# Kernel optimization log

Hardware: AMD Instinct MI355X
Metric: run time of the kernel (lower is better)

## Reference

```python
import jax, jax.numpy as jnp
import numpy as np

SIZE = 11
SIGMA = 1.5
C1 = 0.01 ** 2
C2 = 0.03 ** 2


def gaussian_kernel(size, sigma):
    x, y = np.mgrid[-size:size + 1, -size:size + 1]
    k = np.exp(-0.5 * (x * x + y * y) / (sigma * sigma))
    return (k / k.sum()).astype(np.float32)


def _dwconv(x, w, pad):
    # depthwise conv, NCHW input, OIHW kernel (C,1,kh,kw)
    return jax.lax.conv_general_dilated(
        x, w, window_strides=(1, 1), padding=[(pad, pad), (pad, pad)],
        dimension_numbers=('NCHW', 'OIHW', 'NCHW'),
        feature_group_count=x.shape[1])


def setup_inputs() -> dict:
    key = jax.random.key(0)
    k1, k2 = jax.random.split(key)
    B, C, H, W = 16, 3, 512, 512
    inp = jax.random.uniform(k1, (B, C, H, W), dtype=jnp.float32)
    tgt = jax.random.uniform(k2, (B, C, H, W), dtype=jnp.float32)
    kern = gaussian_kernel(SIZE, SIGMA)  # (23,23)
    weight = jnp.asarray(np.tile(kern, (C, 1, 1, 1)))  # (C,1,23,23)
    return {"input": inp, "target": tgt, "weight": weight}


def reference(input, target, weight):
    pad = SIZE
    mean1 = _dwconv(input, weight, pad)
    mean2 = _dwconv(target, weight, pad)
    mean1_sq = mean1 * mean1
    mean2_sq = mean2 * mean2
    mean_12 = mean1 * mean2
    sigma1_sq = _dwconv(input * input, weight, pad) - mean1_sq
    sigma2_sq = _dwconv(target * target, weight, pad) - mean2_sq
    sigma_12 = _dwconv(input * target, weight, pad) - mean_12
    ssim = (2 * mean_12 + C1) * (2 * sigma_12 + C2) / (
        (mean1_sq + mean2_sq + C1) * (sigma1_sq + sigma2_sq + C2))
    return 1.0 - ssim.mean()
```

## Files before the change

kernel.cpp:

```cpp
#include <hip/hip_runtime.h>
#include <hip/hip_bf16.h>

typedef float f32x4 __attribute__((ext_vector_type(4)));
typedef short bf16x8 __attribute__((ext_vector_type(8)));

#define HH 512
#define WW 512
#define NPLANES 48
#define KSIZE 23
#define NBLK (16 * 16 * NPLANES)
#define C1V 1.0e-4f
#define C2V 9.0e-4f

#define SB_O   0
#define SA_O   3960
#define OV_O   7920
#define G_O    8568
#define HB_O   0
#define HB_CH  2048
#define SPITCH 72
#define LDS_TOT 10616

#define SWZ(rho, k) ((k) ^ (((rho) & 7) << 3))

__device__ __forceinline__ unsigned cvtpk(float a, float b) {
    union { __hip_bfloat162 h; unsigned u; } cv;
    cv.h = __float22bfloat162_rn(make_float2(a, b));
    return cv.u;
}

__device__ __forceinline__ void prod2(unsigned a, unsigned b,
                                      unsigned& pab, unsigned& pss) {
    float al = __uint_as_float(a << 16), ah = __uint_as_float(a & 0xffff0000u);
    float bl = __uint_as_float(b << 16), bh = __uint_as_float(b & 0xffff0000u);
    pab = cvtpk(al * bl, ah * bh);
    pss = cvtpk(al * al + bl * bl, ah * ah + bh * bh);
}

__device__ __forceinline__ f32x4 mfma16(uint4 a, uint4 b, f32x4 c) {
    union { uint4 u; bf16x8 h; } ua, ub;
    ua.u = a; ub.u = b;
    return __builtin_amdgcn_mfma_f32_16x16x32_bf16(ua.h, ub.h, c, 0, 0, 0);
}

__global__ __launch_bounds__(64) void ssim_prep_kernel(
    const float* __restrict__ w, unsigned* __restrict__ Gg)
{
    const int lane = threadIdx.x;
    float gv = 0.f;
    if (lane < KSIZE) {
        #pragma unroll
        for (int k = 0; k < KSIZE; ++k) gv += w[lane * KSIZE + k];
    }
    for (int idx = lane; idx < 32 * 32; idx += 64) {
        int r = idx >> 5, kd = idx & 31;
        int d0 = 2 * kd - 1 - r;
        float g0 = __shfl(gv, d0 & 63, 64);
        float g1 = __shfl(gv, (d0 + 1) & 63, 64);
        g0 = ((unsigned)d0 < (unsigned)KSIZE) ? g0 : 0.f;
        g1 = ((unsigned)(d0 + 1) < (unsigned)KSIZE) ? g1 : 0.f;
        Gg[idx] = cvtpk(g0, g1);
    }
}

__global__ __launch_bounds__(256, 6) void ssim_main_kernel(
    const float* __restrict__ in, const float* __restrict__ tg,
    const unsigned* __restrict__ Gg, float* __restrict__ partial)
{
    __shared__ __align__(16) unsigned short lds[LDS_TOT];
    __shared__ float swsum[4];

    const int tid = threadIdx.x;
    const int wave = tid >> 6, lane = tid & 63;
    const int m = lane & 15, q = lane >> 4;

    const int blk = blockIdx.x;
    const int plane = blk >> 8;
    const int t2 = blk & 255;
    const int x0 = (t2 & 15) * 32 - 12;
    const int y0 = (t2 >> 4) * 32 - 12;
    const float* __restrict__ inp = in + (size_t)plane * (HH * WW);
    const float* __restrict__ tgp = tg + (size_t)plane * (HH * WW);

    const bool interior = (x0 >= 0) && (y0 >= 0) && (x0 + 64 <= WW) && (y0 + 55 <= HH);

    float4 La[2][2], Lb[2][2];
    if (interior) {
        #pragma unroll
        for (int it = 0; it < 2; ++it) {
            int t = tid + it * 256;
            if (t < 440) {
                int r = t >> 3, c8 = (t & 7) << 3;
                const float4* pa = (const float4*)(inp + (y0 + r) * WW + x0 + c8);
                const float4* pb = (const float4*)(tgp + (y0 + r) * WW + x0 + c8);
                La[it][0] = pa[0]; La[it][1] = pa[1];
                Lb[it][0] = pb[0]; Lb[it][1] = pb[1];
            }
        }
    }

    {
        int r = tid >> 3;
        int dc = (tid & 7) << 2;
        uint4 g4 = *(const uint4*)(Gg + r * 32 + dc);
        *(uint4*)&lds[G_O + r * 64 + (((dc << 1)) ^ ((r & 7) << 3))] = g4;
    }
    if (tid < 81) {
        uint4 z; z.x = z.y = z.z = z.w = 0u;
        *(uint4*)&lds[OV_O + tid * 8] = z;
    }

    if (interior) {
        #pragma unroll
        for (int it = 0; it < 2; ++it) {
            int t = tid + it * 256;
            if (t < 440) {
                int r = t >> 3, c8 = (t & 7) << 3;
                uint4 va, vb;
                va.x = cvtpk(La[it][0].x, La[it][0].y); va.y = cvtpk(La[it][0].z, La[it][0].w);
                va.z = cvtpk(La[it][1].x, La[it][1].y); va.w = cvtpk(La[it][1].z, La[it][1].w);
                vb.x = cvtpk(Lb[it][0].x, Lb[it][0].y); vb.y = cvtpk(Lb[it][0].z, Lb[it][0].w);
                vb.z = cvtpk(Lb[it][1].x, Lb[it][1].y); vb.w = cvtpk(Lb[it][1].z, Lb[it][1].w);
                *(uint4*)&lds[SA_O + r * SPITCH + c8] = va;
                *(uint4*)&lds[SB_O + r * SPITCH + c8] = vb;
            }
        }
    } else {
        unsigned* ldsw = (unsigned*)lds;
        for (int t = tid; t < 55 * 32; t += 256) {
            int r = t >> 5, cd = t & 31;
            int gy = y0 + r, gx = x0 + cd * 2;
            float a0 = 0.f, a1 = 0.f, b0 = 0.f, b1 = 0.f;
            if (gy >= 0 && gy < HH) {
                const float* ri = inp + gy * WW;
                const float* rt = tgp + gy * WW;
                if ((unsigned)gx < (unsigned)WW)       { a0 = ri[gx];     b0 = rt[gx]; }
                if ((unsigned)(gx + 1) < (unsigned)WW) { a1 = ri[gx + 1]; b1 = rt[gx + 1]; }
            }
            ldsw[(SA_O >> 1) + r * 36 + cd] = cvtpk(a0, a1);
            ldsw[(SB_O >> 1) + r * 36 + cd] = cvtpk(b0, b1);
        }
    }
    __syncthreads();

    f32x4 acc[4][2];
    const f32x4 zz = {0.f, 0.f, 0.f, 0.f};
    #pragma unroll
    for (int ch = 0; ch < 4; ++ch) { acc[ch][0] = zz; acc[ch][1] = zz; }

    #pragma unroll
    for (int ks = 0; ks < 2; ++ks) {
        const int off = (wave * 16 + m) * SPITCH + ks * 32 + q * 8;
        uint4 ua = *(const uint4*)&lds[SA_O + off];
        uint4 ub = *(const uint4*)&lds[SB_O + off];
        uint4 uab, uss;
        prod2(ua.x, ub.x, uab.x, uss.x);
        prod2(ua.y, ub.y, uab.y, uss.y);
        prod2(ua.z, ub.z, uab.z, uss.z);
        prod2(ua.w, ub.w, uab.w, uss.w);
        #pragma unroll
        for (int nc = 0; nc < 2; ++nc) {
            const int gr = nc * 16 + m;
            uint4 gf = *(const uint4*)&lds[G_O + gr * 64 + SWZ(gr, ks * 32 + q * 8)];
            acc[0][nc] = mfma16(ua,  gf, acc[0][nc]);
            acc[1][nc] = mfma16(ub,  gf, acc[1][nc]);
            acc[2][nc] = mfma16(uss, gf, acc[2][nc]);
            acc[3][nc] = mfma16(uab, gf, acc[3][nc]);
        }
    }
    __syncthreads();

    #pragma unroll
    for (int ch = 0; ch < 4; ++ch)
        #pragma unroll
        for (int nc = 0; nc < 2; ++nc) {
            f32x4 a = acc[ch][nc];
            uint2 pk;
            pk.x = cvtpk(a[0], a[1]);
            pk.y = cvtpk(a[2], a[3]);
            const int col = nc * 16 + m;
            const int rb = wave * 16 + q * 4;
            *(uint2*)&lds[HB_O + ch * HB_CH + col * 64 + SWZ(col, rb)] = pk;
        }
    __syncthreads();

    const int mrow = wave >> 1, nc2 = wave & 1;
    f32x4 av[4];
    #pragma unroll
    for (int ch = 0; ch < 4; ++ch) av[ch] = zz;

    #pragma unroll
    for (int ks = 0; ks < 2; ++ks) {
        const int ar = mrow * 16 + m;
        uint4 ga = *(const uint4*)&lds[G_O + ar * 64 + SWZ(ar, ks * 32 + q * 8)];
        #pragma unroll
        for (int ch = 0; ch < 4; ++ch) {
            const int col = nc2 * 16 + m;
            uint4 ub = *(const uint4*)&lds[HB_O + ch * HB_CH + col * 64 + SWZ(col, ks * 32 + q * 8)];
            av[ch] = mfma16(ga, ub, av[ch]);
        }
    }

    float lsum = 0.f;
    #pragma unroll
    for (int i = 0; i < 4; ++i) {
        float vx = av[0][i], vt = av[1][i];
        float vss = av[2][i], vxt = av[3][i];
        float m1s = vx * vx, m2s = vt * vt, m12 = vx * vt;
        float sss = vss - m1s - m2s;
        float s12 = vxt - m12;
        float num = (2.f * m12 + C1V) * (2.f * s12 + C2V);
        float den = (m1s + m2s + C1V) * (sss + C2V);
        lsum += num * __builtin_amdgcn_rcpf(den);
    }
    #pragma unroll
    for (int off = 32; off > 0; off >>= 1)
        lsum += __shfl_down(lsum, off, 64);
    if (lane == 0) swsum[wave] = lsum;
    __syncthreads();
    if (tid == 0)
        partial[blk] = swsum[0] + swsum[1] + swsum[2] + swsum[3];
}

__global__ __launch_bounds__(256) void ssim_final_kernel(
    const float* __restrict__ partial, float* __restrict__ out)
{
    __shared__ float swsum[4];
    const int tid = threadIdx.x;
    float s = 0.f;
    const float4* p4 = (const float4*)partial;
    for (int i = tid; i < NBLK / 4; i += 256) {
        float4 v = p4[i];
        s += (v.x + v.y) + (v.z + v.w);
    }
    #pragma unroll
    for (int off = 32; off > 0; off >>= 1)
        s += __shfl_down(s, off, 64);
    if ((tid & 63) == 0) swsum[tid >> 6] = s;
    __syncthreads();
    if (tid == 0)
        out[0] = 1.0f - (swsum[0] + swsum[1] + swsum[2] + swsum[3])
                        * (1.0f / ((float)NPLANES * HH * WW));
}

extern "C" void kernel_launch(void* const* d_in, const int* in_sizes, int n_in,
                              void* d_out, int out_size, void* d_ws, size_t ws_size,
                              hipStream_t stream) {
    const float* inp = (const float*)d_in[0];
    const float* tgt = (const float*)d_in[1];
    const float* wgt = (const float*)d_in[2];
    float* out = (float*)d_out;
    float* partial = (float*)d_ws;
    unsigned* Gg = (unsigned*)((char*)d_ws + NBLK * sizeof(float));

    ssim_prep_kernel<<<1, 64, 0, stream>>>(wgt, Gg);
    ssim_main_kernel<<<NBLK, 256, 0, stream>>>(inp, tgt, Gg, partial);
    ssim_final_kernel<<<1, 256, 0, stream>>>(partial, out);
}
```

Before: 157.5 us.

## Fold prep and final reduction kernels into main kernel with atomic last-block reduce

Each block now builds the packed Gaussian weight table in LDS directly from the 23x23 weight tensor instead of reading a table made by a separate prep kernel. The final reduction moves into the main kernel: every block bumps an atomic counter, and the last block to finish sums all partials and writes the result. This drops two kernel launches but adds a memset launch, 23-element weight row sums in every block, and a threadfence plus atomic per block.

```diff
diff --git a/kernel.cpp b/kernel.cpp
--- a/kernel.cpp
+++ b/kernel.cpp
@@ -43,32 +43,14 @@
     return __builtin_amdgcn_mfma_f32_16x16x32_bf16(ua.h, ub.h, c, 0, 0, 0);
 }
 
-__global__ __launch_bounds__(64) void ssim_prep_kernel(
-    const float* __restrict__ w, unsigned* __restrict__ Gg)
-{
-    const int lane = threadIdx.x;
-    float gv = 0.f;
-    if (lane < KSIZE) {
-        #pragma unroll
-        for (int k = 0; k < KSIZE; ++k) gv += w[lane * KSIZE + k];
-    }
-    for (int idx = lane; idx < 32 * 32; idx += 64) {
-        int r = idx >> 5, kd = idx & 31;
-        int d0 = 2 * kd - 1 - r;
-        float g0 = __shfl(gv, d0 & 63, 64);
-        float g1 = __shfl(gv, (d0 + 1) & 63, 64);
-        g0 = ((unsigned)d0 < (unsigned)KSIZE) ? g0 : 0.f;
-        g1 = ((unsigned)(d0 + 1) < (unsigned)KSIZE) ? g1 : 0.f;
-        Gg[idx] = cvtpk(g0, g1);
-    }
-}
-
 __global__ __launch_bounds__(256, 6) void ssim_main_kernel(
     const float* __restrict__ in, const float* __restrict__ tg,
-    const unsigned* __restrict__ Gg, float* __restrict__ partial)
+    const float* __restrict__ w, float* __restrict__ partial,
+    int* __restrict__ counter, float* __restrict__ out)
 {
     __shared__ __align__(16) unsigned short lds[LDS_TOT];
     __shared__ float swsum[4];
+    __shared__ int lastFlag;
 
     const int tid = threadIdx.x;
     const int wave = tid >> 6, lane = tid & 63;
@@ -100,10 +82,24 @@
     }
 
     {
-        int r = tid >> 3;
-        int dc = (tid & 7) << 2;
-        uint4 g4 = *(const uint4*)(Gg + r * 32 + dc);
-        *(uint4*)&lds[G_O + r * 64 + (((dc << 1)) ^ ((r & 7) << 3))] = g4;
+        float gv = 0.f;
+        if (lane < KSIZE) {
+            #pragma unroll
+            for (int k = 0; k < KSIZE; ++k) gv += w[lane * KSIZE + k];
+        }
+        unsigned* gw = (unsigned*)lds + (G_O >> 1);
+        const int kd = lane & 31;
+        const int rh = (lane >> 5) << 2;
+        #pragma unroll
+        for (int i = 0; i < 4; ++i) {
+            int r = wave * 8 + rh + i;
+            int d0 = 2 * kd - 1 - r;
+            float g0 = __shfl(gv, d0 & 63, 64);
+            float g1 = __shfl(gv, (d0 + 1) & 63, 64);
+            g0 = ((unsigned)d0 < (unsigned)KSIZE) ? g0 : 0.f;
+            g1 = ((unsigned)(d0 + 1) < (unsigned)KSIZE) ? g1 : 0.f;
+            gw[r * 32 + (kd ^ ((r & 7) << 2))] = cvtpk(g0, g1);
+        }
     }
     if (tid < 81) {
         uint4 z; z.x = z.y = z.z = z.w = 0u;
@@ -218,29 +214,32 @@
         lsum += __shfl_down(lsum, off, 64);
     if (lane == 0) swsum[wave] = lsum;
     __syncthreads();
-    if (tid == 0)
+
+    if (tid == 0) {
         partial[blk] = swsum[0] + swsum[1] + swsum[2] + swsum[3];
-}
-
-__global__ __launch_bounds__(256) void ssim_final_kernel(
-    const float* __restrict__ partial, float* __restrict__ out)
-{
-    __shared__ float swsum[4];
-    const int tid = threadIdx.x;
-    float s = 0.f;
-    const float4* p4 = (const float4*)partial;
-    for (int i = tid; i < NBLK / 4; i += 256) {
-        float4 v = p4[i];
-        s += (v.x + v.y) + (v.z + v.w);
-    }
-    #pragma unroll
-    for (int off = 32; off > 0; off >>= 1)
-        s += __shfl_down(s, off, 64);
-    if ((tid & 63) == 0) swsum[tid >> 6] = s;
-    __syncthreads();
-    if (tid == 0)
-        out[0] = 1.0f - (swsum[0] + swsum[1] + swsum[2] + swsum[3])
-                        * (1.0f / ((float)NPLANES * HH * WW));
+        __threadfence();
+        int old = atomicAdd(counter, 1);
+        lastFlag = (old == NBLK - 1);
+    }
+    __syncthreads();
+    if (lastFlag) {
+        __threadfence();
+        float s = 0.f;
+        const float4* p4 = (const float4*)partial;
+        for (int i = tid; i < NBLK / 4; i += 256) {
+            float4 v = p4[i];
+            s += (v.x + v.y) + (v.z + v.w);
+        }
+        #pragma unroll
+        for (int off = 32; off > 0; off >>= 1)
+            s += __shfl_down(s, off, 64);
+        __syncthreads();
+        if (lane == 0) swsum[wave] = s;
+        __syncthreads();
+        if (tid == 0)
+            out[0] = 1.0f - (swsum[0] + swsum[1] + swsum[2] + swsum[3])
+                            * (1.0f / ((float)NPLANES * HH * WW));
+    }
 }
 
 extern "C" void kernel_launch(void* const* d_in, const int* in_sizes, int n_in,
@@ -251,9 +250,9 @@
     const float* wgt = (const float*)d_in[2];
     float* out = (float*)d_out;
     float* partial = (float*)d_ws;
-    unsigned* Gg = (unsigned*)((char*)d_ws + NBLK * sizeof(float));
-
-    ssim_prep_kernel<<<1, 64, 0, stream>>>(wgt, Gg);
-    ssim_main_kernel<<<NBLK, 256, 0, stream>>>(inp, tgt, Gg, partial);
-    ssim_final_kernel<<<1, 256, 0, stream>>>(partial, out);
-}
+    int* counter = (int*)((char*)d_ws + NBLK * sizeof(float));
+
+    hipMemsetAsync(counter, 0, sizeof(int), stream);
+    ssim_main_kernel<<<NBLK, 256, 0, stream>>>(inp, tgt, wgt, partial,
+                                               counter, out);
+}
```

Measured after the change: 581.2 us. +269.1%, slower.

## Widen output tile to 64x32 per block with 512 threads

Applied to the files above, without the earlier changes.

Each block now computes a 64-wide by 32-tall output tile using 8 waves instead of a 32x32 tile with 4 waves, which halves the block count. The horizontal halo overhead per output drops because a 96-column input strip (12-pixel halo on each side) is loaded for 64 output columns instead of a 64-column strip for 32. The Gaussian band matrix grows to 64x96, and its XOR swizzle is replaced by a padded pitch. The cost is more LDS per block (about 46 KB) and larger blocks, which may lower occupancy and the number of blocks resident per CU.

```diff
diff --git a/kernel.cpp b/kernel.cpp
--- a/kernel.cpp
+++ b/kernel.cpp
@@ -8,18 +8,19 @@
 #define WW 512
 #define NPLANES 48
 #define KSIZE 23
-#define NBLK (16 * 16 * NPLANES)
+#define NBLK (8 * 16 * NPLANES)
 #define C1V 1.0e-4f
 #define C2V 9.0e-4f
 
-#define SB_O   0
-#define SA_O   3960
-#define OV_O   7920
-#define G_O    8568
-#define HB_O   0
-#define HB_CH  2048
-#define SPITCH 72
-#define LDS_TOT 10616
+#define G_O    0
+#define SB_O   6656
+#define SA_O   12376
+#define OV_O   18096
+#define HB_O   6656
+#define HB_CH  4096
+#define SPITCH 104
+#define SROWS  55
+#define LDS_TOT 23040
 
 #define SWZ(rho, k) ((k) ^ (((rho) & 7) << 3))
 
@@ -43,92 +44,109 @@
     return __builtin_amdgcn_mfma_f32_16x16x32_bf16(ua.h, ub.h, c, 0, 0, 0);
 }
 
-__global__ __launch_bounds__(64) void ssim_prep_kernel(
+__global__ __launch_bounds__(256) void ssim_prep_kernel(
     const float* __restrict__ w, unsigned* __restrict__ Gg)
 {
-    const int lane = threadIdx.x;
+    const int tid = threadIdx.x, lane = tid & 63;
     float gv = 0.f;
     if (lane < KSIZE) {
         #pragma unroll
         for (int k = 0; k < KSIZE; ++k) gv += w[lane * KSIZE + k];
     }
-    for (int idx = lane; idx < 32 * 32; idx += 64) {
-        int r = idx >> 5, kd = idx & 31;
-        int d0 = 2 * kd - 1 - r;
-        float g0 = __shfl(gv, d0 & 63, 64);
-        float g1 = __shfl(gv, (d0 + 1) & 63, 64);
-        g0 = ((unsigned)d0 < (unsigned)KSIZE) ? g0 : 0.f;
-        g1 = ((unsigned)(d0 + 1) < (unsigned)KSIZE) ? g1 : 0.f;
-        Gg[idx] = cvtpk(g0, g1);
-    }
-}
-
-__global__ __launch_bounds__(256, 6) void ssim_main_kernel(
+    const int idx = blockIdx.x * 256 + tid;
+    const int r = idx / 48, kd = idx % 48;
+    const int d0 = 2 * kd - 1 - r;
+    float g0 = __shfl(gv, d0 & 63, 64);
+    float g1 = __shfl(gv, (d0 + 1) & 63, 64);
+    g0 = ((unsigned)d0 < (unsigned)KSIZE) ? g0 : 0.f;
+    g1 = ((unsigned)(d0 + 1) < (unsigned)KSIZE) ? g1 : 0.f;
+    Gg[r * 48 + kd] = cvtpk(g0, g1);
+}
+
+__global__ __launch_bounds__(512, 6) void ssim_main_kernel(
     const float* __restrict__ in, const float* __restrict__ tg,
     const unsigned* __restrict__ Gg, float* __restrict__ partial)
 {
     __shared__ __align__(16) unsigned short lds[LDS_TOT];
-    __shared__ float swsum[4];
+    __shared__ float swsum[8];
 
     const int tid = threadIdx.x;
     const int wave = tid >> 6, lane = tid & 63;
     const int m = lane & 15, q = lane >> 4;
 
     const int blk = blockIdx.x;
-    const int plane = blk >> 8;
-    const int t2 = blk & 255;
-    const int x0 = (t2 & 15) * 32 - 12;
-    const int y0 = (t2 >> 4) * 32 - 12;
+    const int plane = blk >> 7;
+    const int t2 = blk & 127;
+    const int tx = t2 & 7, ty = t2 >> 3;
+    const int x0 = tx * 64 - 12;
+    const int y0 = ty * 32 - 12;
     const float* __restrict__ inp = in + (size_t)plane * (HH * WW);
     const float* __restrict__ tgp = tg + (size_t)plane * (HH * WW);
 
-    const bool interior = (x0 >= 0) && (y0 >= 0) && (x0 + 64 <= WW) && (y0 + 55 <= HH);
+    const bool interior = (x0 >= 0) && (y0 >= 0) &&
+                          (x0 + 96 <= WW) && (y0 + SROWS <= HH);
 
     float4 La[2][2], Lb[2][2];
     if (interior) {
-        #pragma unroll
-        for (int it = 0; it < 2; ++it) {
-            int t = tid + it * 256;
-            if (t < 440) {
-                int r = t >> 3, c8 = (t & 7) << 3;
-                const float4* pa = (const float4*)(inp + (y0 + r) * WW + x0 + c8);
-                const float4* pb = (const float4*)(tgp + (y0 + r) * WW + x0 + c8);
-                La[it][0] = pa[0]; La[it][1] = pa[1];
-                Lb[it][0] = pb[0]; Lb[it][1] = pb[1];
-            }
+        {
+            int r = tid / 12, c8 = (tid % 12) << 3;
+            const float4* pa = (const float4*)(inp + (y0 + r) * WW + x0 + c8);
+            const float4* pb = (const float4*)(tgp + (y0 + r) * WW + x0 + c8);
+            La[0][0] = pa[0]; La[0][1] = pa[1];
+            Lb[0][0] = pb[0]; Lb[0][1] = pb[1];
+        }
+        if (tid < 148) {
+            int t = tid + 512;
+            int r = t / 12, c8 = (t % 12) << 3;
+            const float4* pa = (const float4*)(inp + (y0 + r) * WW + x0 + c8);
+            const float4* pb = (const float4*)(tgp + (y0 + r) * WW + x0 + c8);
+            La[1][0] = pa[0]; La[1][1] = pa[1];
+            Lb[1][0] = pb[0]; Lb[1][1] = pb[1];
         }
     }
 
     {
-        int r = tid >> 3;
-        int dc = (tid & 7) << 2;
-        uint4 g4 = *(const uint4*)(Gg + r * 32 + dc);
-        *(uint4*)&lds[G_O + r * 64 + (((dc << 1)) ^ ((r & 7) << 3))] = g4;
-    }
-    if (tid < 81) {
+        int r = tid / 12, c = tid % 12;
+        uint4 g4 = *(const uint4*)(Gg + r * 48 + c * 4);
+        *(uint4*)&lds[G_O + r * SPITCH + c * 8] = g4;
+        if (tid < 256) {
+            int t = tid + 512;
+            int r2 = t / 12, c2 = t % 12;
+            uint4 h4 = *(const uint4*)(Gg + r2 * 48 + c2 * 4);
+            *(uint4*)&lds[G_O + r2 * SPITCH + c2 * 8] = h4;
+        }
+    }
+    if (tid < 117) {
         uint4 z; z.x = z.y = z.z = z.w = 0u;
         *(uint4*)&lds[OV_O + tid * 8] = z;
     }
 
     if (interior) {
-        #pragma unroll
-        for (int it = 0; it < 2; ++it) {
-            int t = tid + it * 256;
-            if (t < 440) {
-                int r = t >> 3, c8 = (t & 7) << 3;
-                uint4 va, vb;
-                va.x = cvtpk(La[it][0].x, La[it][0].y); va.y = cvtpk(La[it][0].z, La[it][0].w);
-                va.z = cvtpk(La[it][1].x, La[it][1].y); va.w = cvtpk(La[it][1].z, La[it][1].w);
-                vb.x = cvtpk(Lb[it][0].x, Lb[it][0].y); vb.y = cvtpk(Lb[it][0].z, Lb[it][0].w);
-                vb.z = cvtpk(Lb[it][1].x, Lb[it][1].y); vb.w = cvtpk(Lb[it][1].z, Lb[it][1].w);
-                *(uint4*)&lds[SA_O + r * SPITCH + c8] = va;
-                *(uint4*)&lds[SB_O + r * SPITCH + c8] = vb;
-            }
+        {
+            int r = tid / 12, c8 = (tid % 12) << 3;
+            uint4 va, vb;
+            va.x = cvtpk(La[0][0].x, La[0][0].y); va.y = cvtpk(La[0][0].z, La[0][0].w);
+            va.z = cvtpk(La[0][1].x, La[0][1].y); va.w = cvtpk(La[0][1].z, La[0][1].w);
+            vb.x = cvtpk(Lb[0][0].x, Lb[0][0].y); vb.y = cvtpk(Lb[0][0].z, Lb[0][0].w);
+            vb.z = cvtpk(Lb[0][1].x, Lb[0][1].y); vb.w = cvtpk(Lb[0][1].z, Lb[0][1].w);
+            *(uint4*)&lds[SA_O + r * SPITCH + c8] = va;
+            *(uint4*)&lds[SB_O + r * SPITCH + c8] = vb;
+        }
+        if (tid < 148) {
+            int t = tid + 512;
+            int r = t / 12, c8 = (t % 12) << 3;
+            uint4 va, vb;
+            va.x = cvtpk(La[1][0].x, La[1][0].y); va.y = cvtpk(La[1][0].z, La[1][0].w);
+            va.z = cvtpk(La[1][1].x, La[1][1].y); va.w = cvtpk(La[1][1].z, La[1][1].w);
+            vb.x = cvtpk(Lb[1][0].x, Lb[1][0].y); vb.y = cvtpk(Lb[1][0].z, Lb[1][0].w);
+            vb.z = cvtpk(Lb[1][1].x, Lb[1][1].y); vb.w = cvtpk(Lb[1][1].z, Lb[1][1].w);
+            *(uint4*)&lds[SA_O + r * SPITCH + c8] = va;
+            *(uint4*)&lds[SB_O + r * SPITCH + c8] = vb;
         }
     } else {
         unsigned* ldsw = (unsigned*)lds;
-        for (int t = tid; t < 55 * 32; t += 256) {
-            int r = t >> 5, cd = t & 31;
+        for (int t = tid; t < SROWS * 48; t += 512) {
+            int r = t / 48, cd = t % 48;
             int gy = y0 + r, gx = x0 + cd * 2;
             float a0 = 0.f, a1 = 0.f, b0 = 0.f, b1 = 0.f;
             if (gy >= 0 && gy < HH) {
@@ -137,20 +155,22 @@
                 if ((unsigned)gx < (unsigned)WW)       { a0 = ri[gx];     b0 = rt[gx]; }
                 if ((unsigned)(gx + 1) < (unsigned)WW) { a1 = ri[gx + 1]; b1 = rt[gx + 1]; }
             }
-            ldsw[(SA_O >> 1) + r * 36 + cd] = cvtpk(a0, a1);
-            ldsw[(SB_O >> 1) + r * 36 + cd] = cvtpk(b0, b1);
-        }
-    }
-    __syncthreads();
-
+            ldsw[(SA_O >> 1) + r * 52 + cd] = cvtpk(a0, a1);
+            ldsw[(SB_O >> 1) + r * 52 + cd] = cvtpk(b0, b1);
+        }
+    }
+    __syncthreads();
+
+    const int wg = wave >> 2, wt = wave & 3;
     f32x4 acc[4][2];
     const f32x4 zz = {0.f, 0.f, 0.f, 0.f};
     #pragma unroll
     for (int ch = 0; ch < 4; ++ch) { acc[ch][0] = zz; acc[ch][1] = zz; }
 
     #pragma unroll
-    for (int ks = 0; ks < 2; ++ks) {
-        const int off = (wave * 16 + m) * SPITCH + ks * 32 + q * 8;
+    for (int ksi = 0; ksi < 2; ++ksi) {
+        const int ksel = wg + ksi;
+        const int off = (wt * 16 + m) * SPITCH + ksel * 32 + q * 8;
         uint4 ua = *(const uint4*)&lds[SA_O + off];
         uint4 ub = *(const uint4*)&lds[SB_O + off];
         uint4 uab, uss;
@@ -160,8 +180,8 @@
         prod2(ua.w, ub.w, uab.w, uss.w);
         #pragma unroll
         for (int nc = 0; nc < 2; ++nc) {
-            const int gr = nc * 16 + m;
-            uint4 gf = *(const uint4*)&lds[G_O + gr * 64 + SWZ(gr, ks * 32 + q * 8)];
+            const int gr = wg * 32 + nc * 16 + m;
+            uint4 gf = *(const uint4*)&lds[G_O + gr * SPITCH + ksel * 32 + q * 8];
             acc[0][nc] = mfma16(ua,  gf, acc[0][nc]);
             acc[1][nc] = mfma16(ub,  gf, acc[1][nc]);
             acc[2][nc] = mfma16(uss, gf, acc[2][nc]);
@@ -178,21 +198,20 @@
             uint2 pk;
             pk.x = cvtpk(a[0], a[1]);
             pk.y = cvtpk(a[2], a[3]);
-            const int col = nc * 16 + m;
-            const int rb = wave * 16 + q * 4;
+            const int col = wg * 32 + nc * 16 + m;
+            const int rb = wt * 16 + q * 4;
             *(uint2*)&lds[HB_O + ch * HB_CH + col * 64 + SWZ(col, rb)] = pk;
         }
     __syncthreads();
 
-    const int mrow = wave >> 1, nc2 = wave & 1;
+    const int mrow = wave >> 2, nc2 = wave & 3;
     f32x4 av[4];
     #pragma unroll
     for (int ch = 0; ch < 4; ++ch) av[ch] = zz;
 
     #pragma unroll
     for (int ks = 0; ks < 2; ++ks) {
-        const int ar = mrow * 16 + m;
-        uint4 ga = *(const uint4*)&lds[G_O + ar * 64 + SWZ(ar, ks * 32 + q * 8)];
+        uint4 ga = *(const uint4*)&lds[G_O + (mrow * 16 + m) * SPITCH + ks * 32 + q * 8];
         #pragma unroll
         for (int ch = 0; ch < 4; ++ch) {
             const int col = nc2 * 16 + m;
@@ -219,7 +238,8 @@
     if (lane == 0) swsum[wave] = lsum;
     __syncthreads();
     if (tid == 0)
-        partial[blk] = swsum[0] + swsum[1] + swsum[2] + swsum[3];
+        partial[blk] = ((swsum[0] + swsum[1]) + (swsum[2] + swsum[3]))
+                     + ((swsum[4] + swsum[5]) + (swsum[6] + swsum[7]));
 }
 
 __global__ __launch_bounds__(256) void ssim_final_kernel(
@@ -253,7 +273,7 @@
     float* partial = (float*)d_ws;
     unsigned* Gg = (unsigned*)((char*)d_ws + NBLK * sizeof(float));
 
-    ssim_prep_kernel<<<1, 64, 0, stream>>>(wgt, Gg);
-    ssim_main_kernel<<<NBLK, 256, 0, stream>>>(inp, tgt, Gg, partial);
+    ssim_prep_kernel<<<12, 256, 0, stream>>>(wgt, Gg);
+    ssim_main_kernel<<<NBLK, 512, 0, stream>>>(inp, tgt, Gg, partial);
     ssim_final_kernel<<<1, 256, 0, stream>>>(partial, out);
 }
```

After: 167.8 us. 6.6% more time.
